# Kernel optimization log

Measured on AMD Instinct MI355X. Metric: run time of the kernel, lower is better.

## Reference

```python
import jax, jax.numpy as jnp
import numpy as np

TOP_N = 10
N_HEADS = 8

def _layernorm(x, g, b, eps=1e-5):
    mu = jnp.mean(x, axis=-1, keepdims=True)
    var = jnp.mean((x - mu) ** 2, axis=-1, keepdims=True)
    return (x - mu) * jax.lax.rsqrt(var + eps) * g + b

def setup_inputs() -> dict:
    key = jax.random.key(0)
    ks = jax.random.split(key, 16)
    B, N, D = 4096, 32768, 512
    s = 1.0 / np.sqrt(D)
    inp = {
        "visit_rep": jax.random.normal(ks[0], (B, D), jnp.float32),
        "E_mem_patient_rep": jax.random.normal(ks[1], (N, D), jnp.float32),
        "E_mem_med_rep": jax.random.normal(ks[2], (N, D), jnp.float32),
        "Wq": jax.random.uniform(ks[3], (D, D), jnp.float32, -s, s),
        "Wk": jax.random.uniform(ks[4], (D, D), jnp.float32, -s, s),
        "Wv": jax.random.uniform(ks[5], (D, D), jnp.float32, -s, s),
        "bq": jnp.zeros((D,), jnp.float32),
        "bk": jnp.zeros((D,), jnp.float32),
        "bv": jnp.zeros((D,), jnp.float32),
        "Wo": jax.random.uniform(ks[6], (D, D), jnp.float32, -s, s),
        "bo": jnp.zeros((D,), jnp.float32),
        "W1": jax.random.uniform(ks[7], (D, D), jnp.float32, -s, s),
        "b1": jax.random.uniform(ks[8], (D,), jnp.float32, -s, s),
        "W2": jax.random.uniform(ks[9], (D, D), jnp.float32, -s, s),
        "b2": jax.random.uniform(ks[10], (D,), jnp.float32, -s, s),
        "ln1_g": jnp.ones((D,), jnp.float32),
        "ln1_b": jnp.zeros((D,), jnp.float32),
        "ln2_g": jnp.ones((D,), jnp.float32),
        "ln2_b": jnp.zeros((D,), jnp.float32),
    }
    return inp

def reference(visit_rep, E_mem_patient_rep, E_mem_med_rep,
              Wq, bq, Wk, bk, Wv, bv, Wo, bo,
              W1, b1, W2, b2, ln1_g, ln1_b, ln2_g, ln2_b):
    B, D = visit_rep.shape
    H = N_HEADS
    hd = D // H
    # --- exact L2 kNN (faiss GpuIndexFlatL2 equivalent), detached ---
    q = jax.lax.stop_gradient(visit_rep)
    M = jax.lax.stop_gradient(E_mem_patient_rep)
    d2 = (jnp.sum(q * q, axis=1, keepdims=True)
          - 2.0 * q @ M.T
          + jnp.sum(M * M, axis=1)[None, :])          # [B, N]
    _, I = jax.lax.top_k(-d2, TOP_N)                    # [B, top_n]
    k = E_mem_patient_rep[I]                            # [B, top_n, D]
    v = E_mem_med_rep[I]                                # [B, top_n, D]
    # --- multihead attention, query seq-len 1 ---
    qh = (visit_rep @ Wq.T + bq).reshape(B, H, hd)
    kh = (k @ Wk.T + bk).reshape(B, TOP_N, H, hd)
    vh = (v @ Wv.T + bv).reshape(B, TOP_N, H, hd)
    scores = jnp.einsum("bhd,bnhd->bhn", qh, kh) / np.sqrt(hd)
    attn = jax.nn.softmax(scores, axis=-1)
    ctx = jnp.einsum("bhn,bnhd->bhd", attn, vh).reshape(B, D)
    attn_out = ctx @ Wo.T + bo
    # --- residual + norms + FFN (dropout = identity in eval) ---
    x = _layernorm(visit_rep + attn_out, ln1_g, ln1_b)
    ff = (jax.nn.leaky_relu(x @ W1.T + b1, 0.01)) @ W2.T + b2
    x = _layernorm(x + ff, ln2_g, ln2_b)
    return x
```

## Files before the change

kernel.cpp:

```cpp
#include <hip/hip_runtime.h>
#include <math.h>

#define BQ 4096
#define NMEM 32768
#define DD 512
#define TOPN 10
#define NBX 128
#define ENT 2048
#define NCF 16
#define LK 6
#define FINF 3.402823466e+38f
#define IMAX 0x7fffffff

typedef __attribute__((ext_vector_type(8))) short    bf16x8;
typedef __attribute__((ext_vector_type(4))) float    f32x4;
typedef __attribute__((ext_vector_type(4))) int      i32x4;

__device__ __forceinline__ unsigned short f2bf(float x) {
    unsigned int u = __float_as_uint(x);
    u += 0x7fffu + ((u >> 16) & 1u);
    return (unsigned short)(u >> 16);
}
__device__ __forceinline__ void async_copy16(const void* gp, void* lp) {
    __builtin_amdgcn_global_load_lds(
        (const __attribute__((address_space(1))) void*)gp,
        (__attribute__((address_space(3))) void*)lp, 16, 0, 0);
}
__device__ __forceinline__ bool lt_si(float s, int j, float s2, int j2) {
    return (s < s2) || (s == s2 && j < j2);
}
template<int KN>
__device__ __forceinline__ void topk_insert(float (&ts)[KN], int (&ti)[KN], float s, int j) {
    if (!lt_si(s, j, ts[KN-1], ti[KN-1])) return;
    #pragma unroll
    for (int p = KN-1; p > 0; --p) {
        if (lt_si(s, j, ts[p-1], ti[p-1])) { ts[p] = ts[p-1]; ti[p] = ti[p-1]; }
        else { ts[p] = s; ti[p] = j; return; }
    }
    ts[0] = s; ti[0] = j;
}

struct CastDesc {
    const float* in[7];
    unsigned short* out[7];
    int start[8];
};
__global__ __launch_bounds__(256) void cast_multi_kernel(CastDesc d) {
    int blk = blockIdx.x;
    int seg = 0;
    #pragma unroll
    for (int s = 0; s < 6; ++s) seg += (blk >= d.start[s + 1]) ? 1 : 0;
    int local = blk - d.start[seg];
    int i = (local * 256 + threadIdx.x) * 4;
    float4 v = *(const float4*)(d.in[seg] + i);
    ushort4 o;
    o.x = f2bf(v.x); o.y = f2bf(v.y); o.z = f2bf(v.z); o.w = f2bf(v.w);
    *(ushort4*)(d.out[seg] + i) = o;
}

__global__ __launch_bounds__(256) void cast_norm2_kernel(
        const float* __restrict__ inA, unsigned short* __restrict__ outA,
        const float* __restrict__ inB, unsigned short* __restrict__ outB,
        const float* __restrict__ inV,
        signed char* __restrict__ outA8, signed char* __restrict__ outV8,
        float* __restrict__ mnorm, float* __restrict__ msc,
        float* __restrict__ qsc) {
    const int pl = blockIdx.y;
    if (pl == 2 && blockIdx.x >= BQ / 4) return;
    const float* in = (pl == 0) ? inA : (pl == 1 ? inB : inV);
    int row = blockIdx.x * 4 + (threadIdx.x >> 6);
    int lane = threadIdx.x & 63;
    const float* r = in + (size_t)row * DD + lane * 8;
    float4 a = *(const float4*)r;
    float4 b = *(const float4*)(r + 4);
    if (pl < 2) {
        unsigned short* out = pl ? outB : outA;
        ushort4 oa, ob;
        oa.x = f2bf(a.x); oa.y = f2bf(a.y); oa.z = f2bf(a.z); oa.w = f2bf(a.w);
        ob.x = f2bf(b.x); ob.y = f2bf(b.y); ob.z = f2bf(b.z); ob.w = f2bf(b.w);
        unsigned short* op = out + (size_t)row * DD + lane * 8;
        *(ushort4*)op = oa; *(ushort4*)(op + 4) = ob;
    }
    if (pl != 1) {
        float ax = fmaxf(fmaxf(fmaxf(fabsf(a.x), fabsf(a.y)), fmaxf(fabsf(a.z), fabsf(a.w))),
                         fmaxf(fmaxf(fabsf(b.x), fabsf(b.y)), fmaxf(fabsf(b.z), fabsf(b.w))));
        float s = a.x*a.x + a.y*a.y + a.z*a.z + a.w*a.w
                + b.x*b.x + b.y*b.y + b.z*b.z + b.w*b.w;
        #pragma unroll
        for (int off = 32; off; off >>= 1) {
            ax = fmaxf(ax, __shfl_xor(ax, off, 64));
            if (pl == 0) s += __shfl_xor(s, off, 64);
        }
        ax = fmaxf(ax, 1e-30f);
        float inv = 127.0f / ax;
        int q[8];
        q[0] = __float2int_rn(a.x*inv); q[1] = __float2int_rn(a.y*inv);
        q[2] = __float2int_rn(a.z*inv); q[3] = __float2int_rn(a.w*inv);
        q[4] = __float2int_rn(b.x*inv); q[5] = __float2int_rn(b.y*inv);
        q[6] = __float2int_rn(b.z*inv); q[7] = __float2int_rn(b.w*inv);
        unsigned w0 = (q[0]&255) | ((q[1]&255)<<8) | ((q[2]&255)<<16) | ((unsigned)(q[3]&255)<<24);
        unsigned w1 = (q[4]&255) | ((q[5]&255)<<8) | ((q[6]&255)<<16) | ((unsigned)(q[7]&255)<<24);
        signed char* o8 = (pl == 0 ? outA8 : outV8) + (size_t)row * DD + lane * 8;
        *(uint2*)o8 = make_uint2(w0, w1);
        if (lane == 0) {
            if (pl == 0) { mnorm[row] = s; msc[row] = ax * (1.0f/127.0f); }
            else         { qsc[row] = ax * (1.0f/127.0f); }
        }
    }
}

__global__ __launch_bounds__(512, 4) void gemm_knn_kernel(
        const signed char* __restrict__ Q8,
        const signed char* __restrict__ M8,
        const float* __restrict__ mnorm, const float* __restrict__ msc,
        const float* __restrict__ qsc,
        unsigned* __restrict__ cand_part) {
    __shared__ __align__(16) struct {
        signed char A[2][256][64];
        signed char B[2][128][64];
    } sh;
    __shared__ float tb_mn[256], tb_ms2[256], qsl[128];
    const int tid  = threadIdx.x;
    const int lane = tid & 63;
    const int wave = tid >> 6;
    const int quad = lane >> 4, c16 = lane & 15;
    const int wmem = wave >> 1, wq = wave & 1;
    const int mb0 = blockIdx.x * 256;
    const int q0  = blockIdx.y * 128;
    const int srow   = tid >> 2;
    const int schunk = (tid & 3) ^ ((tid >> 3) & 3);
    const signed char* ag = M8 + (size_t)(mb0 + srow) * DD + schunk * 16;
    const signed char* bg = Q8 + (size_t)(q0 + srow) * DD + schunk * 16;
    const int cq = (quad ^ ((c16 >> 1) & 3)) * 16;

    i32x4 acc[4][4] = {};
    i32x4 af[4], bf[4];

    if (tid < 256)      { tb_mn[tid] = mnorm[mb0 + tid]; tb_ms2[tid] = -2.0f * msc[mb0 + tid]; }
    else if (tid < 384) { qsl[tid - 256] = qsc[q0 + tid - 256]; }

#define STG(tt) do {                                                            \
    const int s_ = (tt) & 1;                                                    \
    async_copy16(ag + (size_t)(tt)*64,            &sh.A[s_][srow][(tid & 3) * 16]);      \
    async_copy16(ag + (size_t)(tt)*64 + 128*DD,   &sh.A[s_][128 + srow][(tid & 3) * 16]);\
    async_copy16(bg + (size_t)(tt)*64,            &sh.B[s_][srow][(tid & 3) * 16]);      \
} while (0)
#define RD(tt) do {                                                             \
    const int s_ = (tt) & 1;                                                    \
    _Pragma("unroll")                                                           \
    for (int mt = 0; mt < 4; ++mt)                                              \
        af[mt] = *(const i32x4*)&sh.A[s_][wmem*64 + mt*16 + c16][cq];           \
    _Pragma("unroll")                                                           \
    for (int nt = 0; nt < 4; ++nt)                                              \
        bf[nt] = *(const i32x4*)&sh.B[s_][wq*64 + nt*16 + c16][cq];             \
} while (0)
#define MM() do {                                                               \
    _Pragma("unroll")                                                           \
    for (int mt = 0; mt < 4; ++mt)                                              \
        _Pragma("unroll")                                                       \
        for (int nt = 0; nt < 4; ++nt)                                          \
            acc[mt][nt] = __builtin_amdgcn_mfma_i32_16x16x64_i8(                \
                af[mt], bf[nt], acc[mt][nt], 0, 0, 0);                          \
} while (0)

    STG(0);
    asm volatile("s_waitcnt vmcnt(0)" ::: "memory");
    __builtin_amdgcn_s_barrier();
    __builtin_amdgcn_sched_barrier(0);

    #pragma unroll
    for (int t = 0; t < 8; ++t) {
        RD(t);
        if (t < 7) STG(t + 1);
        __builtin_amdgcn_sched_barrier(0);
        asm volatile("s_waitcnt lgkmcnt(0)" ::: "memory");
        __builtin_amdgcn_sched_barrier(0);
        __builtin_amdgcn_s_setprio(1);
        MM();
        __builtin_amdgcn_s_setprio(0);
        __builtin_amdgcn_sched_barrier(0);
        asm volatile("s_waitcnt vmcnt(0)" ::: "memory");
        __builtin_amdgcn_sched_barrier(0);
        __builtin_amdgcn_s_barrier();
    }
#undef STG
#undef RD
#undef MM

    #pragma unroll
    for (int nt = 0; nt < 4; ++nt) {
        float qv = qsl[wq*64 + nt*16 + c16];
        unsigned s0, s1, s2, s3;
        #pragma unroll
        for (int mt = 0; mt < 4; ++mt) {
            unsigned k0, k1, k2, k3, lo, hi;
            {
                unsigned kk[4];
                #pragma unroll
                for (int r = 0; r < 4; ++r) {
                    int mrow = wmem*64 + mt*16 + quad*4 + r;
                    float s = fmaxf(fmaf(tb_ms2[mrow] * qv, (float)acc[mt][nt][r], tb_mn[mrow]), 0.f);
                    kk[r] = (__float_as_uint(s) & 0xFFFFFF80u)
                          | (unsigned)(((wmem & 1) << 6) | (mt*16 + quad*4 + r));
                }
                k0 = kk[0]; k1 = kk[1]; k2 = kk[2]; k3 = kk[3];
            }
            lo = min(k0,k1); hi = max(k0,k1); k0 = lo; k1 = hi;
            lo = min(k2,k3); hi = max(k2,k3); k2 = lo; k3 = hi;
            lo = min(k0,k2); hi = max(k0,k2); k0 = lo; k2 = hi;
            lo = min(k1,k3); hi = max(k1,k3); k1 = lo; k3 = hi;
            lo = min(k1,k2); hi = max(k1,k2); k1 = lo; k2 = hi;
            if (mt == 0) { s0 = k0; s1 = k1; s2 = k2; s3 = k3; }
            else {
                unsigned b0 = min(s0,k3), b1 = min(s1,k2), b2 = min(s2,k1), b3 = min(s3,k0);
                unsigned t0 = min(b0,b2), t2 = max(b0,b2), t1 = min(b1,b3), t3 = max(b1,b3);
                s0 = min(t0,t1); s1 = max(t0,t1); s2 = min(t2,t3); s3 = max(t2,t3);
            }
        }
        unsigned p0, p1, p2, p3, b0, b1, b2, b3, t0, t1, t2, t3;
        p0 = (unsigned)__shfl_xor((int)s0, 16, 64);
        p1 = (unsigned)__shfl_xor((int)s1, 16, 64);
        p2 = (unsigned)__shfl_xor((int)s2, 16, 64);
        p3 = (unsigned)__shfl_xor((int)s3, 16, 64);
        b0 = min(s0,p3); b1 = min(s1,p2); b2 = min(s2,p1); b3 = min(s3,p0);
        t0 = min(b0,b2); t2 = max(b0,b2); t1 = min(b1,b3); t3 = max(b1,b3);
        s0 = min(t0,t1); s1 = max(t0,t1); s2 = min(t2,t3); s3 = max(t2,t3);
        p0 = (unsigned)__shfl_xor((int)s0, 32, 64);
        p1 = (unsigned)__shfl_xor((int)s1, 32, 64);
        p2 = (unsigned)__shfl_xor((int)s2, 32, 64);
        p3 = (unsigned)__shfl_xor((int)s3, 32, 64);
        b0 = min(s0,p3); b1 = min(s1,p2); b2 = min(s2,p1); b3 = min(s3,p0);
        if (quad == 0) {
            *(uint4*)(cand_part + (size_t)(q0 + wq*64 + nt*16 + c16) * ENT
                      + blockIdx.x * 16 + wmem * 4) = make_uint4(b0, b1, b2, b3);
        }
    }
}

__global__ __launch_bounds__(256) void knn_select_kernel(
        const unsigned* __restrict__ cand_part,
        const float* __restrict__ Q, const float* __restrict__ Mm,
        const float* __restrict__ mnorm,
        int* __restrict__ knn_idx) {
    const int row = blockIdx.x;
    const int wave = threadIdx.x >> 6, lane = threadIdx.x & 63;
    __shared__ unsigned sk[64];
    __shared__ int      sc[64];
    __shared__ int      ids[NCF];
    __shared__ float    d2s[NCF];

    unsigned ks[LK]; int ti[LK];
    #pragma unroll
    for (int q = 0; q < LK; ++q) { ks[q] = 0xFFFFFFFFu; ti[q] = IMAX; }
    const uint4* p4 = (const uint4*)(cand_part + (size_t)row * ENT) + wave * 128;
    #pragma unroll
    for (int i = 0; i < 2; ++i) {
        uint4 v = p4[lane + 64 * i];
        #pragma unroll
        for (int e = 0; e < 4; ++e) {
            unsigned k = (&v.x)[e];
            int pos = wave * 512 + (lane + 64 * i) * 4 + e;
            int gcol = (pos >> 3) * 128 + (int)(k & 127u);
            bool cm[LK];
            #pragma unroll
            for (int q = 0; q < LK; ++q) cm[q] = k < ks[q];
            #pragma unroll
            for (int q = LK - 1; q > 0; --q) {
                unsigned tns = cm[q] ? k : ks[q];  int tni = cm[q] ? gcol : ti[q];
                ks[q] = cm[q-1] ? ks[q-1] : tns;
                ti[q] = cm[q-1] ? ti[q-1] : tni;
            }
            ks[0] = cm[0] ? k : ks[0];
            ti[0] = cm[0] ? gcol : ti[0];
        }
    }
    #pragma unroll
    for (int r = 0; r < NCF; ++r) {
        unsigned mk = ks[0]; int mi = ti[0];
        #pragma unroll
        for (int off = 1; off < 64; off <<= 1) {
            unsigned ok = (unsigned)__shfl_xor((int)mk, off, 64);
            int      oi = __shfl_xor(mi, off, 64);
            bool t = (ok < mk) || (ok == mk && oi < mi);
            mk = t ? ok : mk; mi = t ? oi : mi;
        }
        bool win = (ks[0] == mk) && (ti[0] == mi);
        #pragma unroll
        for (int q = 0; q < LK - 1; ++q) {
            ks[q] = win ? ks[q+1] : ks[q];
            ti[q] = win ? ti[q+1] : ti[q];
        }
        ks[LK-1] = win ? 0xFFFFFFFFu : ks[LK-1];
        ti[LK-1] = win ? IMAX : ti[LK-1];
        if (lane == r) { sk[wave * NCF + r] = mk; sc[wave * NCF + r] = mi; }
    }
    __syncthreads();
    if (wave == 0) {
        unsigned myk = sk[lane];
        int      myc = sc[lane];
        #pragma unroll
        for (int r = 0; r < NCF; ++r) {
            unsigned mk = myk; int mi = myc;
            #pragma unroll
            for (int off = 1; off < 64; off <<= 1) {
                unsigned ok = (unsigned)__shfl_xor((int)mk, off, 64);
                int      oi = __shfl_xor(mi, off, 64);
                bool t = (ok < mk) || (ok == mk && oi < mi);
                mk = t ? ok : mk; mi = t ? oi : mi;
            }
            bool win = (myk == mk) && (myc == mi);
            myk = win ? 0xFFFFFFFFu : myk;
            myc = win ? IMAX : myc;
            if (lane == r) ids[r] = mi;
        }
    }
    __syncthreads();
    float4 q0 = *(const float4*)(Q + (size_t)row * DD + lane * 8);
    float4 q1 = *(const float4*)(Q + (size_t)row * DD + lane * 8 + 4);
    for (int c = wave; c < NCF; c += 4) {
        int j = ids[c];
        const float* mr = Mm + (size_t)j * DD;
        float4 m0 = *(const float4*)(mr + lane * 8);
        float4 m1 = *(const float4*)(mr + lane * 8 + 4);
        float dot = q0.x*m0.x + q0.y*m0.y + q0.z*m0.z + q0.w*m0.w
                  + q1.x*m1.x + q1.y*m1.y + q1.z*m1.z + q1.w*m1.w;
        #pragma unroll
        for (int off = 32; off; off >>= 1) dot += __shfl_xor(dot, off, 64);
        if (lane == 0) d2s[c] = fmaf(-2.f, dot, mnorm[j]);
    }
    __syncthreads();
    if (threadIdx.x == 0) {
        float ts[TOPN]; int tj[TOPN];
        #pragma unroll
        for (int p = 0; p < TOPN; ++p) { ts[p] = FINF; tj[p] = IMAX; }
        for (int c = 0; c < NCF; ++c) topk_insert<TOPN>(ts, tj, d2s[c], ids[c]);
        #pragma unroll
        for (int p = 0; p < TOPN; ++p) knn_idx[row * TOPN + p] = tj[p];
    }
}

template<int ACT, int OUT_BF16>
__global__ __launch_bounds__(256) void gemm_bf16_nt(
        const unsigned short* __restrict__ A,
        const unsigned short* __restrict__ B,
        const float* __restrict__ bias,
        void* __restrict__ Cout, int ldc) {
    __shared__ __align__(16) unsigned short As[128 * 64];
    __shared__ __align__(16) unsigned short Bs[128 * 64];
    const int tid  = threadIdx.x;
    const int wave = tid >> 6, lane = tid & 63;
    const int quad = lane >> 4, c16 = lane & 15;
    const int m0 = blockIdx.y * 128, n0 = blockIdx.x * 128;
    const int wm0 = (wave >> 1) * 64, wn0 = (wave & 1) * 64;
    const int srow = wave * 32 + (lane >> 3);
    const int schunk = (lane & 7) ^ ((lane >> 3) & 7);
    const int xsw = c16 & 7;

    f32x4 acc[4][4] = {};

    for (int kt = 0; kt < DD; kt += 64) {
        __syncthreads();
        #pragma unroll
        for (int i = 0; i < 4; ++i) {
            const unsigned short* ga = A + (size_t)(m0 + srow + i * 8) * DD + kt + schunk * 8;
            async_copy16(ga, &As[(wave * 32 + i * 8) * 64]);
            const unsigned short* gb = B + (size_t)(n0 + srow + i * 8) * DD + kt + schunk * 8;
            async_copy16(gb, &Bs[(wave * 32 + i * 8) * 64]);
        }
        __syncthreads();
        #pragma unroll
        for (int ks = 0; ks < 64; ks += 32) {
            const int coff = (((ks >> 3) + quad) ^ xsw) << 3;
            bf16x8 af[4], bff[4];
            #pragma unroll
            for (int mt = 0; mt < 4; ++mt)
                af[mt] = *(const bf16x8*)&As[(wm0 + mt * 16 + c16) * 64 + coff];
            #pragma unroll
            for (int nt = 0; nt < 4; ++nt)
                bff[nt] = *(const bf16x8*)&Bs[(wn0 + nt * 16 + c16) * 64 + coff];
            #pragma unroll
            for (int mt = 0; mt < 4; ++mt)
                #pragma unroll
                for (int nt = 0; nt < 4; ++nt)
                    acc[mt][nt] = __builtin_amdgcn_mfma_f32_16x16x32_bf16(
                        af[mt], bff[nt], acc[mt][nt], 0, 0, 0);
        }
    }
    #pragma unroll
    for (int nt = 0; nt < 4; ++nt) {
        int ncol = n0 + wn0 + nt * 16 + c16;
        float bv = bias[ncol];
        #pragma unroll
        for (int mt = 0; mt < 4; ++mt) {
            size_t rbase = (size_t)(m0 + wm0 + mt * 16 + quad * 4) * ldc + ncol;
            #pragma unroll
            for (int r = 0; r < 4; ++r) {
                float v = acc[mt][nt][r] + bv;
                if (ACT == 1) v = v >= 0.f ? v : 0.01f * v;
                if (OUT_BF16) ((unsigned short*)Cout)[rbase + (size_t)r * ldc] = f2bf(v);
                else          ((float*)Cout)[rbase + (size_t)r * ldc] = v;
            }
        }
    }
}

struct G3 {
    const unsigned short* A[3];
    const unsigned short* B[3];
    const float* bias[3];
    void* C[3];
    int obf[3];
};
__global__ __launch_bounds__(256) void gemm3_kernel(G3 g) {
    const int yy = blockIdx.y;
    const int z = (yy >= 512) ? 2 : (yy >= 256 ? 1 : 0);
    const int my = yy - z * 256;
    __shared__ __align__(16) unsigned short As[128 * 64];
    __shared__ __align__(16) unsigned short Bs[128 * 64];
    const unsigned short* A = g.A[z];
    const unsigned short* B = g.B[z];
    const int tid  = threadIdx.x;
    const int wave = tid >> 6, lane = tid & 63;
    const int quad = lane >> 4, c16 = lane & 15;
    const int m0 = my * 128, n0 = blockIdx.x * 128;
    const int wm0 = (wave >> 1) * 64, wn0 = (wave & 1) * 64;
    const int srow = wave * 32 + (lane >> 3);
    const int schunk = (lane & 7) ^ ((lane >> 3) & 7);
    const int xsw = c16 & 7;

    f32x4 acc[4][4] = {};

    for (int kt = 0; kt < DD; kt += 64) {
        __syncthreads();
        #pragma unroll
        for (int i = 0; i < 4; ++i) {
            const unsigned short* ga = A + (size_t)(m0 + srow + i * 8) * DD + kt + schunk * 8;
            async_copy16(ga, &As[(wave * 32 + i * 8) * 64]);
            const unsigned short* gb = B + (size_t)(n0 + srow + i * 8) * DD + kt + schunk * 8;
            async_copy16(gb, &Bs[(wave * 32 + i * 8) * 64]);
        }
        __syncthreads();
        #pragma unroll
        for (int ks = 0; ks < 64; ks += 32) {
            const int coff = (((ks >> 3) + quad) ^ xsw) << 3;
            bf16x8 af[4], bff[4];
            #pragma unroll
            for (int mt = 0; mt < 4; ++mt)
                af[mt] = *(const bf16x8*)&As[(wm0 + mt * 16 + c16) * 64 + coff];
            #pragma unroll
            for (int nt = 0; nt < 4; ++nt)
                bff[nt] = *(const bf16x8*)&Bs[(wn0 + nt * 16 + c16) * 64 + coff];
            #pragma unroll
            for (int mt = 0; mt < 4; ++mt)
                #pragma unroll
                for (int nt = 0; nt < 4; ++nt)
                    acc[mt][nt] = __builtin_amdgcn_mfma_f32_16x16x32_bf16(
                        af[mt], bff[nt], acc[mt][nt], 0, 0, 0);
        }
    }
    const int obf = g.obf[z];
    #pragma unroll
    for (int nt = 0; nt < 4; ++nt) {
        int ncol = n0 + wn0 + nt * 16 + c16;
        float bv = g.bias[z][ncol];
        #pragma unroll
        for (int mt = 0; mt < 4; ++mt) {
            size_t rbase = (size_t)(m0 + wm0 + mt * 16 + quad * 4) * DD + ncol;
            #pragma unroll
            for (int r = 0; r < 4; ++r) {
                float v = acc[mt][nt][r] + bv;
                if (obf) ((unsigned short*)g.C[z])[rbase + (size_t)r * DD] = f2bf(v);
                else     ((float*)g.C[z])[rbase + (size_t)r * DD] = v;
            }
        }
    }
}

__global__ __launch_bounds__(512) void attn_kernel(
        const float* __restrict__ qh, const unsigned short* __restrict__ Kall,
        const unsigned short* __restrict__ Vall, const int* __restrict__ knn_idx,
        unsigned short* __restrict__ ctx_b) {
    const int b = blockIdx.x;
    const int h = threadIdx.x >> 6;
    const int l = threadIdx.x & 63;
    const int col = (h << 6) + l;
    int idxs[TOPN];
    #pragma unroll
    for (int n = 0; n < TOPN; ++n) idxs[n] = knn_idx[b * TOPN + n];
    const float q = qh[(size_t)b * DD + col];
    float sc[TOPN];
    #pragma unroll
    for (int n = 0; n < TOPN; ++n) {
        float p = q * __uint_as_float((unsigned)Kall[(size_t)idxs[n] * DD + col] << 16);
        #pragma unroll
        for (int off = 32; off; off >>= 1) p += __shfl_xor(p, off, 64);
        sc[n] = p * 0.125f;
    }
    float mx = sc[0];
    #pragma unroll
    for (int n = 1; n < TOPN; ++n) mx = fmaxf(mx, sc[n]);
    float se = 0.f;
    #pragma unroll
    for (int n = 0; n < TOPN; ++n) { sc[n] = expf(sc[n] - mx); se += sc[n]; }
    const float inv = 1.f / se;
    float o = 0.f;
    #pragma unroll
    for (int n = 0; n < TOPN; ++n)
        o = fmaf(sc[n] * inv,
                 __uint_as_float((unsigned)Vall[(size_t)idxs[n] * DD + col] << 16), o);
    ctx_b[(size_t)b * DD + col] = f2bf(o);
}

template<int EMIT_BF16>
__global__ __launch_bounds__(256) void add_ln_kernel(
        const float* __restrict__ X, const float* __restrict__ Y,
        const float* __restrict__ g, const float* __restrict__ be,
        float* __restrict__ out, unsigned short* __restrict__ out_b) {
    const int row = blockIdx.x;
    const int t = threadIdx.x;
    const size_t base = (size_t)row * DD;
    float v0 = X[base + t]       + Y[base + t];
    float v1 = X[base + 256 + t] + Y[base + 256 + t];
    float s = v0 + v1, sq = v0 * v0 + v1 * v1;
    #pragma unroll
    for (int off = 32; off; off >>= 1) { s += __shfl_xor(s, off, 64); sq += __shfl_xor(sq, off, 64); }
    __shared__ float rs[4], rq[4];
    const int w = t >> 6, l = t & 63;
    if (l == 0) { rs[w] = s; rq[w] = sq; }
    __syncthreads();
    float tot  = rs[0] + rs[1] + rs[2] + rs[3];
    float totq = rq[0] + rq[1] + rq[2] + rq[3];
    float mu = tot * (1.f / DD);
    float var = totq * (1.f / DD) - mu * mu;
    float rstd = rsqrtf(var + 1e-5f);
    float o0 = (v0 - mu) * rstd * g[t]       + be[t];
    float o1 = (v1 - mu) * rstd * g[256 + t] + be[256 + t];
    out[base + t] = o0;
    out[base + 256 + t] = o1;
    if (EMIT_BF16) {
        out_b[base + t] = f2bf(o0);
        out_b[base + 256 + t] = f2bf(o1);
    }
}

extern "C" void kernel_launch(void* const* d_in, const int* in_sizes, int n_in,
                              void* d_out, int out_size, void* d_ws, size_t ws_size,
                              hipStream_t stream) {
    const float* visit = (const float*)d_in[0];
    const float* Epat  = (const float*)d_in[1];
    const float* Emed  = (const float*)d_in[2];
    const float* Wq = (const float*)d_in[3];
    const float* Wk = (const float*)d_in[4];
    const float* Wv = (const float*)d_in[5];
    const float* bq = (const float*)d_in[6];
    const float* bk = (const float*)d_in[7];
    const float* bv = (const float*)d_in[8];
    const float* Wo = (const float*)d_in[9];
    const float* bo = (const float*)d_in[10];
    const float* W1 = (const float*)d_in[11];
    const float* b1 = (const float*)d_in[12];
    const float* W2 = (const float*)d_in[13];
    const float* b2 = (const float*)d_in[14];
    const float* ln1g = (const float*)d_in[15];
    const float* ln1b = (const float*)d_in[16];
    const float* ln2g = (const float*)d_in[17];
    const float* ln2b = (const float*)d_in[18];
    float* out = (float*)d_out;

    char* base = (char*)d_ws;
    const size_t MB = 1u << 20;
    float* mnorm   = (float*)(base);
    float* msc     = (float*)(base + 256*1024);
    float* qsc     = (float*)(base + 512*1024);
    int*   knn_idx = (int*)  (base + 2*MB);
    float* qh      = (float*)(base + 3*MB);
    float* attn_o  = qh;
    float* x1      = (float*)(base + 11*MB);
    float* ff      = (float*)(base + 19*MB);
    unsigned short* Qb    = (unsigned short*)(base + 27*MB);
    unsigned short* ctx_b = (unsigned short*)(base + 31*MB);
    unsigned short* x1_b  = (unsigned short*)(base + 35*MB);
    unsigned short* h1_b  = (unsigned short*)(base + 39*MB);
    unsigned short* Wq_b  = (unsigned short*)(base + 43*MB);
    unsigned short* Wk_b  = Wq_b + 262144;
    unsigned short* Wv_b  = Wk_b + 262144;
    unsigned short* Wo_b  = Wv_b + 262144;
    unsigned short* W1_b  = Wo_b + 262144;
    unsigned short* W2_b  = W1_b + 262144;
    unsigned short* Mb     = (unsigned short*)(base + 46*MB);
    unsigned short* Emed_b = (unsigned short*)(base + 78*MB);
    unsigned short* Kall = (unsigned short*)(base + 110*MB);
    unsigned short* Vall = Kall + (size_t)NMEM * DD;
    unsigned* cand_part = (unsigned*)Kall;
    signed char* M8 = (signed char*)(base + 142*MB);
    signed char* Q8 = (signed char*)(base + 158*MB);

    cast_norm2_kernel<<<dim3(NMEM / 4, 3), 256, 0, stream>>>(
        Epat, Mb, Emed, Emed_b, visit, M8, Q8, mnorm, msc, qsc);
    CastDesc cd;
    cd.in[0] = visit; cd.out[0] = Qb;
    cd.in[1] = Wq; cd.in[2] = Wk; cd.in[3] = Wv; cd.in[4] = Wo; cd.in[5] = W1; cd.in[6] = W2;
    cd.out[1] = Wq_b; cd.out[2] = Wk_b; cd.out[3] = Wv_b; cd.out[4] = Wo_b; cd.out[5] = W1_b; cd.out[6] = W2_b;
    cd.start[0] = 0; cd.start[1] = 2048;
    for (int s = 2; s <= 7; ++s) cd.start[s] = cd.start[s-1] + 256;
    cast_multi_kernel<<<cd.start[7], 256, 0, stream>>>(cd);

    gemm_knn_kernel<<<dim3(NBX, BQ / 128), 512, 0, stream>>>(Q8, M8, mnorm, msc, qsc, cand_part);
    knn_select_kernel<<<BQ, 256, 0, stream>>>(cand_part, visit, Epat, mnorm, knn_idx);

    G3 g3;
    g3.A[0] = Mb;     g3.B[0] = Wk_b; g3.bias[0] = bk; g3.C[0] = Kall; g3.obf[0] = 1;
    g3.A[1] = Emed_b; g3.B[1] = Wv_b; g3.bias[1] = bv; g3.C[1] = Vall; g3.obf[1] = 1;
    g3.A[2] = Qb;     g3.B[2] = Wq_b; g3.bias[2] = bq; g3.C[2] = qh;   g3.obf[2] = 0;
    gemm3_kernel<<<dim3(4, 544), 256, 0, stream>>>(g3);

    attn_kernel<<<BQ, 512, 0, stream>>>(qh, Kall, Vall, knn_idx, ctx_b);

    gemm_bf16_nt<0,0><<<dim3(4, BQ / 128), 256, 0, stream>>>(ctx_b, Wo_b, bo, attn_o, DD);
    add_ln_kernel<1><<<BQ, 256, 0, stream>>>(visit, attn_o, ln1g, ln1b, x1, x1_b);
    gemm_bf16_nt<1,1><<<dim3(4, BQ / 128), 256, 0, stream>>>(x1_b, W1_b, b1, h1_b, DD);
    gemm_bf16_nt<0,0><<<dim3(4, BQ / 128), 256, 0, stream>>>(h1_b, W2_b, b2, ff,   DD);
    add_ln_kernel<0><<<BQ, 256, 0, stream>>>(x1, ff, ln2g, ln2b, out, nullptr);
}
```

Measured before the change: 495.3 us.

## Triple-buffer kNN GEMM and restructure projection GEMM into pipelined 256x128 tiles

The int8 kNN distance GEMM moves from double to triple buffering of LDS tiles, so global loads run two stages ahead. The K/V/Q projection GEMM is rewritten to use 512-thread blocks with 256x128 tiles, 32-wide K steps and a three-stage async-copy pipeline, replacing its synchronous load-then-compute loop. The attention kernel now processes two batch rows per block. Together these aim to hide memory latency behind MFMA work, at the cost of more LDS per block and possibly lower occupancy.

```diff
diff --git a/kernel.cpp b/kernel.cpp
--- a/kernel.cpp
+++ b/kernel.cpp
@@ -116,8 +116,8 @@
         const float* __restrict__ qsc,
         unsigned* __restrict__ cand_part) {
     __shared__ __align__(16) struct {
-        signed char A[2][256][64];
-        signed char B[2][128][64];
+        signed char A[3][256][64];
+        signed char B[3][128][64];
     } sh;
     __shared__ float tb_mn[256], tb_ms2[256], qsl[128];
     const int tid  = threadIdx.x;
@@ -140,13 +140,13 @@
     else if (tid < 384) { qsl[tid - 256] = qsc[q0 + tid - 256]; }
 
 #define STG(tt) do {                                                            \
-    const int s_ = (tt) & 1;                                                    \
+    const int s_ = (tt) % 3;                                                    \
     async_copy16(ag + (size_t)(tt)*64,            &sh.A[s_][srow][(tid & 3) * 16]);      \
     async_copy16(ag + (size_t)(tt)*64 + 128*DD,   &sh.A[s_][128 + srow][(tid & 3) * 16]);\
     async_copy16(bg + (size_t)(tt)*64,            &sh.B[s_][srow][(tid & 3) * 16]);      \
 } while (0)
 #define RD(tt) do {                                                             \
-    const int s_ = (tt) & 1;                                                    \
+    const int s_ = (tt) % 3;                                                    \
     _Pragma("unroll")                                                           \
     for (int mt = 0; mt < 4; ++mt)                                              \
         af[mt] = *(const i32x4*)&sh.A[s_][wmem*64 + mt*16 + c16][cq];           \
@@ -163,15 +163,15 @@
                 af[mt], bf[nt], acc[mt][nt], 0, 0, 0);                          \
 } while (0)
 
-    STG(0);
-    asm volatile("s_waitcnt vmcnt(0)" ::: "memory");
+    STG(0); STG(1);
+    asm volatile("s_waitcnt vmcnt(3)" ::: "memory");
     __builtin_amdgcn_s_barrier();
     __builtin_amdgcn_sched_barrier(0);
 
     #pragma unroll
     for (int t = 0; t < 8; ++t) {
         RD(t);
-        if (t < 7) STG(t + 1);
+        if (t + 2 < 8) STG(t + 2);
         __builtin_amdgcn_sched_barrier(0);
         asm volatile("s_waitcnt lgkmcnt(0)" ::: "memory");
         __builtin_amdgcn_sched_barrier(0);
@@ -179,7 +179,8 @@
         MM();
         __builtin_amdgcn_s_setprio(0);
         __builtin_amdgcn_sched_barrier(0);
-        asm volatile("s_waitcnt vmcnt(0)" ::: "memory");
+        if (t < 6)       asm volatile("s_waitcnt vmcnt(3)" ::: "memory");
+        else if (t == 6) asm volatile("s_waitcnt vmcnt(0)" ::: "memory");
         __builtin_amdgcn_sched_barrier(0);
         __builtin_amdgcn_s_barrier();
     }
@@ -411,61 +412,89 @@
     void* C[3];
     int obf[3];
 };
-__global__ __launch_bounds__(256) void gemm3_kernel(G3 g) {
+__global__ __launch_bounds__(512, 4) void gemm3_kernel(G3 g) {
+    __shared__ __align__(16) struct {
+        unsigned short A[3][256][32];
+        unsigned short B[3][128][32];
+    } sh;
     const int yy = blockIdx.y;
-    const int z = (yy >= 512) ? 2 : (yy >= 256 ? 1 : 0);
-    const int my = yy - z * 256;
-    __shared__ __align__(16) unsigned short As[128 * 64];
-    __shared__ __align__(16) unsigned short Bs[128 * 64];
+    const int z = (yy >= 256) ? 2 : (yy >= 128 ? 1 : 0);
+    const int my = yy - (z == 2 ? 256 : z * 128);
     const unsigned short* A = g.A[z];
     const unsigned short* B = g.B[z];
     const int tid  = threadIdx.x;
-    const int wave = tid >> 6, lane = tid & 63;
+    const int lane = tid & 63;
+    const int wave = tid >> 6;
     const int quad = lane >> 4, c16 = lane & 15;
-    const int m0 = my * 128, n0 = blockIdx.x * 128;
-    const int wm0 = (wave >> 1) * 64, wn0 = (wave & 1) * 64;
-    const int srow = wave * 32 + (lane >> 3);
-    const int schunk = (lane & 7) ^ ((lane >> 3) & 7);
-    const int xsw = c16 & 7;
-
-    f32x4 acc[4][4] = {};
-
-    for (int kt = 0; kt < DD; kt += 64) {
-        __syncthreads();
-        #pragma unroll
-        for (int i = 0; i < 4; ++i) {
-            const unsigned short* ga = A + (size_t)(m0 + srow + i * 8) * DD + kt + schunk * 8;
-            async_copy16(ga, &As[(wave * 32 + i * 8) * 64]);
-            const unsigned short* gb = B + (size_t)(n0 + srow + i * 8) * DD + kt + schunk * 8;
-            async_copy16(gb, &Bs[(wave * 32 + i * 8) * 64]);
-        }
-        __syncthreads();
-        #pragma unroll
-        for (int ks = 0; ks < 64; ks += 32) {
-            const int coff = (((ks >> 3) + quad) ^ xsw) << 3;
-            bf16x8 af[4], bff[4];
-            #pragma unroll
-            for (int mt = 0; mt < 4; ++mt)
-                af[mt] = *(const bf16x8*)&As[(wm0 + mt * 16 + c16) * 64 + coff];
-            #pragma unroll
-            for (int nt = 0; nt < 4; ++nt)
-                bff[nt] = *(const bf16x8*)&Bs[(wn0 + nt * 16 + c16) * 64 + coff];
-            #pragma unroll
-            for (int mt = 0; mt < 4; ++mt)
-                #pragma unroll
-                for (int nt = 0; nt < 4; ++nt)
-                    acc[mt][nt] = __builtin_amdgcn_mfma_f32_16x16x32_bf16(
-                        af[mt], bff[nt], acc[mt][nt], 0, 0, 0);
-        }
-    }
+    const int wm = wave >> 1, wn = wave & 1;
+    const int m0 = my * 256, n0 = blockIdx.x * 128;
+    const int srow   = tid >> 2;
+    const int schunk = (tid & 3) ^ ((tid >> 3) & 3);
+    const unsigned short* ag = A + (size_t)(m0 + srow) * DD + schunk * 8;
+    const unsigned short* bg = B + (size_t)(n0 + srow) * DD + schunk * 8;
+    const int cq = (quad ^ ((c16 >> 1) & 3)) * 8;
+
+    f32x4  acc[4][4] = {};
+    bf16x8 af[4], bf[4];
+
+#define STG(tt) do {                                                            \
+    const int s_ = (tt) % 3;                                                    \
+    async_copy16(ag + (size_t)(tt)*32,            &sh.A[s_][srow][(tid & 3) * 8]);      \
+    async_copy16(ag + (size_t)(tt)*32 + 128*DD,   &sh.A[s_][128 + srow][(tid & 3) * 8]);\
+    async_copy16(bg + (size_t)(tt)*32,            &sh.B[s_][srow][(tid & 3) * 8]);      \
+} while (0)
+#define RD(tt) do {                                                             \
+    const int s_ = (tt) % 3;                                                    \
+    _Pragma("unroll")                                                           \
+    for (int mt = 0; mt < 4; ++mt)                                              \
+        af[mt] = *(const bf16x8*)&sh.A[s_][wm*64 + mt*16 + c16][cq];            \
+    _Pragma("unroll")                                                           \
+    for (int nt = 0; nt < 4; ++nt)                                              \
+        bf[nt] = *(const bf16x8*)&sh.B[s_][wn*64 + nt*16 + c16][cq];            \
+} while (0)
+#define MM() do {                                                               \
+    _Pragma("unroll")                                                           \
+    for (int mt = 0; mt < 4; ++mt)                                              \
+        _Pragma("unroll")                                                       \
+        for (int nt = 0; nt < 4; ++nt)                                          \
+            acc[mt][nt] = __builtin_amdgcn_mfma_f32_16x16x32_bf16(              \
+                af[mt], bf[nt], acc[mt][nt], 0, 0, 0);                          \
+} while (0)
+
+    STG(0); STG(1);
+    asm volatile("s_waitcnt vmcnt(3)" ::: "memory");
+    __builtin_amdgcn_s_barrier();
+    __builtin_amdgcn_sched_barrier(0);
+
+    #pragma unroll
+    for (int t = 0; t < 16; ++t) {
+        RD(t);
+        if (t + 2 < 16) STG(t + 2);
+        __builtin_amdgcn_sched_barrier(0);
+        asm volatile("s_waitcnt lgkmcnt(0)" ::: "memory");
+        __builtin_amdgcn_sched_barrier(0);
+        __builtin_amdgcn_s_setprio(1);
+        MM();
+        __builtin_amdgcn_s_setprio(0);
+        __builtin_amdgcn_sched_barrier(0);
+        if (t < 14)       asm volatile("s_waitcnt vmcnt(3)" ::: "memory");
+        else if (t == 14) asm volatile("s_waitcnt vmcnt(0)" ::: "memory");
+        __builtin_amdgcn_sched_barrier(0);
+        __builtin_amdgcn_s_barrier();
+    }
+#undef STG
+#undef RD
+#undef MM
+
     const int obf = g.obf[z];
+    const float* bias = g.bias[z];
     #pragma unroll
     for (int nt = 0; nt < 4; ++nt) {
-        int ncol = n0 + wn0 + nt * 16 + c16;
-        float bv = g.bias[z][ncol];
+        int ncol = n0 + wn*64 + nt*16 + c16;
+        float bv = bias[ncol];
         #pragma unroll
         for (int mt = 0; mt < 4; ++mt) {
-            size_t rbase = (size_t)(m0 + wm0 + mt * 16 + quad * 4) * DD + ncol;
+            size_t rbase = (size_t)(m0 + wm*64 + mt*16 + quad*4) * DD + ncol;
             #pragma unroll
             for (int r = 0; r < 4; ++r) {
                 float v = acc[mt][nt][r] + bv;
@@ -480,35 +509,38 @@
         const float* __restrict__ qh, const unsigned short* __restrict__ Kall,
         const unsigned short* __restrict__ Vall, const int* __restrict__ knn_idx,
         unsigned short* __restrict__ ctx_b) {
-    const int b = blockIdx.x;
     const int h = threadIdx.x >> 6;
     const int l = threadIdx.x & 63;
     const int col = (h << 6) + l;
-    int idxs[TOPN];
-    #pragma unroll
-    for (int n = 0; n < TOPN; ++n) idxs[n] = knn_idx[b * TOPN + n];
-    const float q = qh[(size_t)b * DD + col];
-    float sc[TOPN];
-    #pragma unroll
-    for (int n = 0; n < TOPN; ++n) {
-        float p = q * __uint_as_float((unsigned)Kall[(size_t)idxs[n] * DD + col] << 16);
-        #pragma unroll
-        for (int off = 32; off; off >>= 1) p += __shfl_xor(p, off, 64);
-        sc[n] = p * 0.125f;
-    }
-    float mx = sc[0];
-    #pragma unroll
-    for (int n = 1; n < TOPN; ++n) mx = fmaxf(mx, sc[n]);
-    float se = 0.f;
-    #pragma unroll
-    for (int n = 0; n < TOPN; ++n) { sc[n] = expf(sc[n] - mx); se += sc[n]; }
-    const float inv = 1.f / se;
-    float o = 0.f;
-    #pragma unroll
-    for (int n = 0; n < TOPN; ++n)
-        o = fmaf(sc[n] * inv,
-                 __uint_as_float((unsigned)Vall[(size_t)idxs[n] * DD + col] << 16), o);
-    ctx_b[(size_t)b * DD + col] = f2bf(o);
+    #pragma unroll
+    for (int e = 0; e < 2; ++e) {
+        const int b = blockIdx.x * 2 + e;
+        int idxs[TOPN];
+        #pragma unroll
+        for (int n = 0; n < TOPN; ++n) idxs[n] = knn_idx[b * TOPN + n];
+        const float q = qh[(size_t)b * DD + col];
+        float sc[TOPN];
+        #pragma unroll
+        for (int n = 0; n < TOPN; ++n) {
+            float p = q * __uint_as_float((unsigned)Kall[(size_t)idxs[n] * DD + col] << 16);
+            #pragma unroll
+            for (int off = 32; off; off >>= 1) p += __shfl_xor(p, off, 64);
+            sc[n] = p * 0.125f;
+        }
+        float mx = sc[0];
+        #pragma unroll
+        for (int n = 1; n < TOPN; ++n) mx = fmaxf(mx, sc[n]);
+        float se = 0.f;
+        #pragma unroll
+        for (int n = 0; n < TOPN; ++n) { sc[n] = expf(sc[n] - mx); se += sc[n]; }
+        const float inv = 1.f / se;
+        float o = 0.f;
+        #pragma unroll
+        for (int n = 0; n < TOPN; ++n)
+            o = fmaf(sc[n] * inv,
+                     __uint_as_float((unsigned)Vall[(size_t)idxs[n] * DD + col] << 16), o);
+        ctx_b[(size_t)b * DD + col] = f2bf(o);
+    }
 }
 
 template<int EMIT_BF16>
@@ -612,9 +644,9 @@
     g3.A[0] = Mb;     g3.B[0] = Wk_b; g3.bias[0] = bk; g3.C[0] = Kall; g3.obf[0] = 1;
     g3.A[1] = Emed_b; g3.B[1] = Wv_b; g3.bias[1] = bv; g3.C[1] = Vall; g3.obf[1] = 1;
     g3.A[2] = Qb;     g3.B[2] = Wq_b; g3.bias[2] = bq; g3.C[2] = qh;   g3.obf[2] = 0;
-    gemm3_kernel<<<dim3(4, 544), 256, 0, stream>>>(g3);
-
-    attn_kernel<<<BQ, 512, 0, stream>>>(qh, Kall, Vall, knn_idx, ctx_b);
+    gemm3_kernel<<<dim3(4, 272), 512, 0, stream>>>(g3);
+
+    attn_kernel<<<BQ / 2, 512, 0, stream>>>(qh, Kall, Vall, knn_idx, ctx_b);
 
     gemm_bf16_nt<0,0><<<dim3(4, BQ / 128), 256, 0, stream>>>(ctx_b, Wo_b, bo, attn_o, DD);
     add_ln_kernel<1><<<BQ, 256, 0, stream>>>(visit, attn_o, ln1g, ln1b, x1, x1_b);
```

New measurement: 497.4 us. No clear change (+0.4%).
